# Kernel tuning notes

Hardware: AMD Instinct MI355X
Metric: run time of the kernel (lower is better)

## Reference

```python
import jax, jax.numpy as jnp
import numpy as np
from jax.scipy.special import ndtr, ndtri

B, N, K = 64, 4096, 128
MU, SIGMA = 0.0, 1.0
_TINY = 1e-7


def setup_inputs() -> dict:
    key = jax.random.key(0)
    k1, k2, k3 = jax.random.split(key, 3)
    C = jax.random.randint(k1, (B, N), 0, K)                      # labels [B,N]
    eps = jax.random.normal(k2, (B, N), dtype=jnp.float32)        # std-normal noise for upper bounds
    U = jax.random.uniform(k3, (B, N, K), dtype=jnp.float32)      # uniforms for inverse-CDF truncnorm
    return {
        "C": C,
        "eps": eps,
        "U": U,
        "mu": jnp.full((1,), MU, dtype=jnp.float32),
        "sigma": jnp.full((1,), SIGMA, dtype=jnp.float32),
    }


def reference(C, eps, U, mu, sigma):
    # Relabel ground-truth labels to 0..K-1 (torch.unique(..., return_inverse=True))
    _, C_new = jnp.unique(C, return_inverse=True)
    C_new = C_new.reshape(C.shape)                                # [B,N]
    Kdim = U.shape[-1]
    # upper bound per (b,i): u ~ N(mu, sigma), reparameterized
    u = mu.reshape(()) + sigma.reshape(()) * eps                  # [B,N]
    # truncnorm.rvs(-inf, u) via inverse CDF: z = Phi^{-1}(U * Phi(u))
    Uc = jnp.clip(U, _TINY, 1.0 - _TINY)
    Z = ndtri(Uc * ndtr(u)[..., None])                            # [B,N,K]
    # Z[b,i,C_new[b,i]] = u[b,i]
    onehot = C_new[..., None] == jnp.arange(Kdim)                 # [B,N,K] bool
    return jnp.where(onehot, u[..., None], Z)
```

## Files before the change

### kernel.cpp

```cpp
#include <hip/hip_runtime.h>
#include <math.h>


typedef float vfloat4 __attribute__((ext_vector_type(4)));

__device__ __forceinline__ float ndtri_fast(float p) {
    const float omp  = 1.0f - p;
    const bool upper = p > 0.5f;
    const float pm   = upper ? omp : p;
    const bool tail  = pm < 0.02425f;

    float qt = sqrtf(-2.0f * __logf(pm));
    float numT = -0.007784894002430293f;
    numT = fmaf(numT, qt, -0.3223964580411365f);
    numT = fmaf(numT, qt, -2.400758277161838f);
    numT = fmaf(numT, qt, -2.549732539343734f);
    numT = fmaf(numT, qt,  4.374664141464968f);
    numT = fmaf(numT, qt,  2.938163982698783f);
    float denT = 0.007784695709041462f;
    denT = fmaf(denT, qt, 0.3224671290700398f);
    denT = fmaf(denT, qt, 2.445134137142996f);
    denT = fmaf(denT, qt, 3.754408661907416f);
    denT = fmaf(denT, qt, 1.0f);

    float qc = p - 0.5f;
    float r  = qc * qc;
    float numC = -39.69683028665376f;
    numC = fmaf(numC, r,  220.9460984245205f);
    numC = fmaf(numC, r, -275.9285104469687f);
    numC = fmaf(numC, r,  138.3577518672690f);
    numC = fmaf(numC, r,  -30.66479806614716f);
    numC = fmaf(numC, r,    2.506628277459239f);
    float denC = -54.47609879822406f;
    denC = fmaf(denC, r,  161.5858368580409f);
    denC = fmaf(denC, r, -155.6989798598866f);
    denC = fmaf(denC, r,   66.80131188771972f);
    denC = fmaf(denC, r,  -13.28068155288572f);
    denC = fmaf(denC, r,    1.0f);

    float num = tail ? numT : numC;
    float den = tail ? denT : denC;
    float s   = tail ? (upper ? -1.0f : 1.0f) : qc;
    return s * num * __builtin_amdgcn_rcpf(den);
}

__device__ __forceinline__ void set_label_bit(int c, unsigned& m0, unsigned& m1,
                                              unsigned& m2, unsigned& m3) {
    unsigned bit = 1u << (c & 31);
    int w = (c >> 5) & 3;
    if      (w == 0) m0 |= bit;
    else if (w == 1) m1 |= bit;
    else if (w == 2) m2 |= bit;
    else             m3 |= bit;
}

__global__ void __launch_bounds__(256) bitmap_kernel(
    const int* __restrict__ C,
    unsigned* __restrict__ mask,
    int n)
{
    __shared__ unsigned sm[4];
    if (threadIdx.x < 4) sm[threadIdx.x] = 0u;
    __syncthreads();

    int i = blockIdx.x * blockDim.x + threadIdx.x;
    int base = i << 2;
    unsigned m0 = 0, m1 = 0, m2 = 0, m3 = 0;

    if (base + 3 < n) {
        int4 c = *reinterpret_cast<const int4*>(C + base);
        set_label_bit(c.x, m0, m1, m2, m3);
        set_label_bit(c.y, m0, m1, m2, m3);
        set_label_bit(c.z, m0, m1, m2, m3);
        set_label_bit(c.w, m0, m1, m2, m3);
    } else {
        for (int j = base; j < n && j < base + 4; ++j)
            set_label_bit(C[j], m0, m1, m2, m3);
    }

    #pragma unroll
    for (int off = 32; off > 0; off >>= 1) {
        m0 |= __shfl_down(m0, off, 64);
        m1 |= __shfl_down(m1, off, 64);
        m2 |= __shfl_down(m2, off, 64);
        m3 |= __shfl_down(m3, off, 64);
    }
    if ((threadIdx.x & 63) == 0) {
        if (m0) atomicOr(&sm[0], m0);
        if (m1) atomicOr(&sm[1], m1);
        if (m2) atomicOr(&sm[2], m2);
        if (m3) atomicOr(&sm[3], m3);
    }
    __syncthreads();
    if (threadIdx.x < 4) {
        unsigned v = sm[threadIdx.x];
        if (v) atomicOr(&mask[threadIdx.x], v);
    }
}

__global__ void __launch_bounds__(256) map_kernel(
    const int* __restrict__ C,
    const float* __restrict__ eps,
    const float* __restrict__ mu_p,
    const float* __restrict__ sigma_p,
    const float4* __restrict__ U4,
    const uint4* __restrict__ mask4,
    float4* __restrict__ out4,
    int total4)
{
    int idx = blockIdx.x * blockDim.x + threadIdx.x;
    if (idx >= total4) return;
    int row = idx >> 5;
    int k0  = (idx & 31) << 2;

    float4 Uv = U4[idx];
    float  e  = eps[row];
    int    c  = C[row];
    uint4  w  = *mask4;

    const float sg = sigma_p[0];
    const float mu = mu_p[0];
    float u   = fmaf(sg, e, mu);
    float phi = 0.5f * erfcf(-u * 0.7071067811865476f);

    int cw = c >> 5;
    unsigned below = (1u << (c & 31)) - 1u;
    int rank = __popc(w.x & ((0 < cw) ? 0xFFFFFFFFu : ((0 == cw) ? below : 0u)))
             + __popc(w.y & ((1 < cw) ? 0xFFFFFFFFu : ((1 == cw) ? below : 0u)))
             + __popc(w.z & ((2 < cw) ? 0xFFFFFFFFu : ((2 == cw) ? below : 0u)))
             + __popc(w.w & ((3 < cw) ? 0xFFFFFFFFu : ((3 == cw) ? below : 0u)));

    const float lo = 1e-7f;
    const float hi = 0.99999988079071045f;

    float p0 = __builtin_amdgcn_fmed3f(Uv.x, lo, hi) * phi;
    float p1 = __builtin_amdgcn_fmed3f(Uv.y, lo, hi) * phi;
    float p2 = __builtin_amdgcn_fmed3f(Uv.z, lo, hi) * phi;
    float p3 = __builtin_amdgcn_fmed3f(Uv.w, lo, hi) * phi;

    float z0 = ndtri_fast(p0);
    float z1 = ndtri_fast(p1);
    float z2 = ndtri_fast(p2);
    float z3 = ndtri_fast(p3);

    vfloat4 o;
    o.x = (k0 + 0 == rank) ? u : z0;
    o.y = (k0 + 1 == rank) ? u : z1;
    o.z = (k0 + 2 == rank) ? u : z2;
    o.w = (k0 + 3 == rank) ? u : z3;

    __builtin_nontemporal_store(o, reinterpret_cast<vfloat4*>(&out4[idx]));
}

extern "C" void kernel_launch(void* const* d_in, const int* in_sizes, int n_in,
                              void* d_out, int out_size, void* d_ws, size_t ws_size,
                              hipStream_t stream) {
    const int*   C     = (const int*)d_in[0];
    const float* eps   = (const float*)d_in[1];
    const float4* U4   = (const float4*)d_in[2];
    const float* mu    = (const float*)d_in[3];
    const float* sigma = (const float*)d_in[4];
    float4* out4 = (float4*)d_out;

    unsigned* mask = (unsigned*)d_ws;

    int n = in_sizes[0];
    int total4 = out_size / 4;

    (void)hipMemsetAsync(d_ws, 0, 4 * sizeof(unsigned), stream);

    int n4 = (n + 3) >> 2;
    int bb = (n4 + 255) / 256;
    bitmap_kernel<<<bb, 256, 0, stream>>>(C, mask, n);

    int mb = (total4 + 255) / 256;
    map_kernel<<<mb, 256, 0, stream>>>(C, eps, mu, sigma, U4,
                                       (const uint4*)mask, out4, total4);
}
```

Before: 243.1 us.

## Replace global atomic label bitmap with per-block slots and drop memset

The label-presence bitmap is now built by a fixed grid of 16 grid-stride blocks, each writing its partial mask to its own workspace slot instead of atomically OR-ing into a zeroed global mask. This removes the hipMemsetAsync launch and the global atomics. In exchange, every thread of the map kernel now loads and ORs 16 uint4 slots, adding cached loads per thread in the large kernel.

```diff
diff --git a/kernel.cpp b/kernel.cpp
--- a/kernel.cpp
+++ b/kernel.cpp
@@ -54,29 +54,31 @@
     else             m3 |= bit;
 }
 
+#define BITMAP_BLOCKS 16
+
 __global__ void __launch_bounds__(256) bitmap_kernel(
     const int* __restrict__ C,
-    unsigned* __restrict__ mask,
+    uint4* __restrict__ slots,
     int n)
 {
     __shared__ unsigned sm[4];
     if (threadIdx.x < 4) sm[threadIdx.x] = 0u;
     __syncthreads();
 
-    int i = blockIdx.x * blockDim.x + threadIdx.x;
-    int base = i << 2;
     unsigned m0 = 0, m1 = 0, m2 = 0, m3 = 0;
 
-    if (base + 3 < n) {
-        int4 c = *reinterpret_cast<const int4*>(C + base);
+    int n4 = n >> 2;
+    int stride = BITMAP_BLOCKS * 256;
+    for (int i = blockIdx.x * 256 + threadIdx.x; i < n4; i += stride) {
+        int4 c = *reinterpret_cast<const int4*>(C + (i << 2));
         set_label_bit(c.x, m0, m1, m2, m3);
         set_label_bit(c.y, m0, m1, m2, m3);
         set_label_bit(c.z, m0, m1, m2, m3);
         set_label_bit(c.w, m0, m1, m2, m3);
-    } else {
-        for (int j = base; j < n && j < base + 4; ++j)
-            set_label_bit(C[j], m0, m1, m2, m3);
     }
+    for (int j = (n4 << 2) + blockIdx.x * 256 + threadIdx.x; j < n;
+         j += stride)
+        set_label_bit(C[j], m0, m1, m2, m3);
 
     #pragma unroll
     for (int off = 32; off > 0; off >>= 1) {
@@ -92,9 +94,10 @@
         if (m3) atomicOr(&sm[3], m3);
     }
     __syncthreads();
-    if (threadIdx.x < 4) {
-        unsigned v = sm[threadIdx.x];
-        if (v) atomicOr(&mask[threadIdx.x], v);
+    if (threadIdx.x == 0) {
+        uint4 v;
+        v.x = sm[0]; v.y = sm[1]; v.z = sm[2]; v.w = sm[3];
+        slots[blockIdx.x] = v;
     }
 }
 
@@ -104,7 +107,7 @@
     const float* __restrict__ mu_p,
     const float* __restrict__ sigma_p,
     const float4* __restrict__ U4,
-    const uint4* __restrict__ mask4,
+    const uint4* __restrict__ slots,
     float4* __restrict__ out4,
     int total4)
 {
@@ -116,7 +119,13 @@
     float4 Uv = U4[idx];
     float  e  = eps[row];
     int    c  = C[row];
-    uint4  w  = *mask4;
+
+    uint4 w = slots[0];
+    #pragma unroll
+    for (int s = 1; s < BITMAP_BLOCKS; ++s) {
+        uint4 t = slots[s];
+        w.x |= t.x; w.y |= t.y; w.z |= t.z; w.w |= t.w;
+    }
 
     const float sg = sigma_p[0];
     const float mu = mu_p[0];
@@ -162,18 +171,14 @@
     const float* sigma = (const float*)d_in[4];
     float4* out4 = (float4*)d_out;
 
-    unsigned* mask = (unsigned*)d_ws;
+    uint4* slots = (uint4*)d_ws;
 
     int n = in_sizes[0];
     int total4 = out_size / 4;
 
-    (void)hipMemsetAsync(d_ws, 0, 4 * sizeof(unsigned), stream);
-
-    int n4 = (n + 3) >> 2;
-    int bb = (n4 + 255) / 256;
-    bitmap_kernel<<<bb, 256, 0, stream>>>(C, mask, n);
+    bitmap_kernel<<<BITMAP_BLOCKS, 256, 0, stream>>>(C, slots, n);
 
     int mb = (total4 + 255) / 256;
     map_kernel<<<mb, 256, 0, stream>>>(C, eps, mu, sigma, U4,
-                                       (const uint4*)mask, out4, total4);
+                                       slots, out4, total4);
 }
```

After: 266.6 us. +9.7%, slower.
